# Performance work log

Hardware: AMD Instinct MI355X
Metric: run time of the kernel (lower is better)

Reference implementation:

```python
import jax, jax.numpy as jnp
import numpy as np
from jax import lax

CUTOFF = 0.25
SIGMA = 1.0
RADIUS = 4  # skimage/scipy default truncate=4.0 -> radius = round(4.0*sigma)


def _gauss_kernel(sigma=SIGMA, radius=RADIUS):
    x = np.arange(-radius, radius + 1, dtype=np.float32)
    k = np.exp(-0.5 * (x / sigma) ** 2)
    return jnp.asarray(k / k.sum())


def _blur_axis(x, axis, kernel):
    r = (kernel.shape[0] - 1) // 2
    pad = [(0, 0)] * x.ndim
    pad[axis] = (r, r)
    xp = jnp.pad(x, pad, mode='edge')  # scipy mode='nearest'
    out = jnp.zeros_like(x)
    for i in range(kernel.shape[0]):  # fixed small tap loop (9 taps)
        out = out + kernel[i] * lax.slice_in_dim(xp, i, i + x.shape[axis], axis=axis)
    return out


def gaussian_smoothing_4d(x):
    # skimage.filters.gaussian on a 4D array smooths over ALL axes (B, C, H, W)
    k = _gauss_kernel().astype(x.dtype)
    for ax in range(4):
        x = _blur_axis(x, ax, k)
    return x


def dht_2d(x):
    # real(FFT(x)) - imag(FFT(flip(x)))
    return (jnp.fft.fftn(x, axes=(2, 3)).real
            - jnp.fft.fftn(jnp.flip(x, axis=(2, 3)), axes=(2, 3)).imag).astype(x.dtype)


def _neg_k(a):
    # X_H(-k): flip both spatial mode axes, then roll by 1 (DC stays put)
    return jnp.roll(jnp.flip(a, axis=(-2, -1)), shift=(1, 1), axis=(-2, -1))


def compl_mul2d(x1, x2):
    x1n, x2n = _neg_k(x1), _neg_k(x2)
    e = lambda a, b: jnp.einsum('bixy,ioxy->boxy', a, b)
    return 0.5 * (e(x1, x2) - e(x1n, x2n) + e(x1, x2n) + e(x1n, x2))


def setup_inputs() -> dict:
    key = jax.random.key(0)
    k1, k2 = jax.random.split(key)
    B, Cin, Cout, H, W, M1, M2 = 16, 64, 64, 128, 128, 20, 20
    x = jax.random.normal(k1, (B, Cin, H, W), dtype=jnp.float32)
    scale = 1.0 / (Cin * Cout)
    w1 = scale * jax.random.uniform(k2, (Cin, Cout, M1, M2), dtype=jnp.float32)
    return {'x': x, 'w1': w1}


def reference(x, w1):
    B, _, H, W = x.shape
    Cout, M1, M2 = w1.shape[1], w1.shape[2], w1.shape[3]
    x_ht = dht_2d(x)
    out_ht = jnp.zeros((B, Cout, H, W), dtype=x.dtype)
    out_ht = out_ht.at[:, :, :M1, :M2].set(
        compl_mul2d(x_ht[:, :, :M1, :M2], w1))
    # inverse DHT = DHT / (H*W)
    y = dht_2d(out_ht) / (H * W)
    y = gaussian_smoothing_4d(y)
    # low-pass mask along last dim only (as in the original)
    freqs = jnp.fft.fftfreq(W)
    mask = (jnp.abs(freqs) <= CUTOFF).astype(y.dtype)
    return y * mask
```

## Files before the change

### kernel.cpp

```cpp
#include <hip/hip_runtime.h>


#define TWO_PI 6.283185307179586f
#define THETA (TWO_PI / 128.0f)

__device__ __forceinline__ void gauss9(float* g) {
  float s = 0.f;
#pragma unroll
  for (int t = 0; t < 9; ++t) { float d = (float)(t - 4); g[t] = expf(-0.5f * d * d); s += g[t]; }
  float inv = 1.f / s;
#pragma unroll
  for (int t = 0; t < 9; ++t) g[t] *= inv;
}

__global__ void __launch_bounds__(256, 4) kBig(
    const float* __restrict__ x, const float* __restrict__ w1,
    float* __restrict__ X1, float* __restrict__ wbT,
    float* __restrict__ L2g, float* __restrict__ RB2g) {
  __shared__ float lds[10240];
  int tid = threadIdx.x;
  int blk = blockIdx.x;

  if (blk < 448) {
    int c = blk / 7, chunk = blk % 7;
    int m0 = chunk * 64;
    int mw = 400 - m0; if (mw > 64) mw = 64;
    for (int t = tid; t < 4096; t += 256) {
      int o = t >> 6, mm = t & 63;
      lds[o * 69 + mm] = (mm < mw) ? w1[(c * 64 + o) * 400 + m0 + mm] : 0.f;
    }
    __syncthreads();
    float g[9]; gauss9(g);
    for (int t = tid; t < 4096; t += 256) {
      int mm = t >> 6, o = t & 63;
      if (mm >= mw) continue;
      float acc = 0.f;
#pragma unroll
      for (int tp = 0; tp < 9; ++tp) {
        int oc = o - 4 + tp; oc = oc < 0 ? 0 : (oc > 63 ? 63 : oc);
        acc += g[tp] * lds[oc * 69 + mm];
      }
      wbT[(c * 400 + m0 + mm) * 64 + o] = acc;
    }
    return;
  }
  if (blk == 448) {
    for (int i = tid; i < 5376; i += 256) {
      int u = i / 42, t = i - u * 42;
      int A = (t < 21) ? t : t - 21;
      float a = (float)((u * A) & 127) * THETA;
      lds[u * 44 + t] = (t < 21) ? cosf(a) : sinf(a);
    }
    __syncthreads();
    float g[9]; gauss9(g);
    for (int i = tid; i < 5376; i += 256) {
      int u = i / 42, t = i - u * 42;
      float acc = 0.f;
#pragma unroll
      for (int tp = 0; tp < 9; ++tp) {
        int uc = u - 4 + tp; uc = uc < 0 ? 0 : (uc > 127 ? 127 : uc);
        acc += g[tp] * lds[uc * 44 + t];
      }
      L2g[t * 128 + u] = acc;
      bool keep = (u <= 32) || (u >= 96);
      RB2g[t * 128 + u] = keep ? acc : 0.f;
    }
    return;
  }

  int bc0 = (blk - 449) * 2;
  const float* xb0 = x + (long)bc0 * 16384;
  const float* xb1 = xb0 + 16384;

  for (int i = tid; i < 2560; i += 256) {
    int n2 = i / 20, k2 = i - n2 * 20;
    float s, c;
    sincosf((float)((k2 * n2) & 127) * THETA, &s, &c);
    lds[n2 * 40 + k2] = c;
    lds[n2 * 40 + 20 + k2] = s;
  }

  int rg = tid & 31, cg = tid >> 5;
  int r0 = rg * 4, c0 = cg * 5;
  float acc0[4][5], acc1[4][5];
#pragma unroll
  for (int i = 0; i < 4; ++i)
#pragma unroll
    for (int j = 0; j < 5; ++j) { acc0[i][j] = 0.f; acc1[i][j] = 0.f; }

  float* xs0 = lds + 5120;
  float* xs1 = lds + 7232;
  for (int ch = 0; ch < 8; ++ch) {
    __syncthreads();
#pragma unroll 4
    for (int it = 0; it < 4; ++it) {
      int t = tid + it * 256;
      int n2l = t & 15, n1g = (t >> 4) & 31, im = t >> 9;
      const float* gp = (im ? xb1 : xb0) + n1g * 512 + ch * 16 + n2l;
      float4 v = make_float4(gp[0], gp[128], gp[256], gp[384]);
      float* dst = im ? xs1 : xs0;
      *(float4*)&dst[n2l * 132 + n1g * 4] = v;
    }
    __syncthreads();
#pragma unroll 4
    for (int k = 0; k < 16; ++k) {
      float4 a0 = *(const float4*)&xs0[k * 132 + r0];
      float4 a1 = *(const float4*)&xs1[k * 132 + r0];
      const float* tr = lds + (ch * 16 + k) * 40 + c0;
      float bv[5] = {tr[0], tr[1], tr[2], tr[3], tr[4]};
      float a0v[4] = {a0.x, a0.y, a0.z, a0.w};
      float a1v[4] = {a1.x, a1.y, a1.z, a1.w};
#pragma unroll
      for (int i = 0; i < 4; ++i)
#pragma unroll
        for (int j = 0; j < 5; ++j) {
          acc0[i][j] += a0v[i] * bv[j];
          acc1[i][j] += a1v[i] * bv[j];
        }
    }
  }
  __syncthreads();
  for (int i = tid; i < 2560; i += 256) {
    int k1 = i >> 7, t = i & 127;
    float s, c;
    sincosf((float)((k1 * t) & 127) * THETA, &s, &c);
    lds[k1 * 128 + (t ^ ((k1 & 7) << 2))] = c;
    lds[(20 + k1) * 128 + (t ^ (((20 + k1) & 7) << 2))] = s;
  }
#pragma unroll
  for (int j = 0; j < 5; ++j) {
    int col = c0 + j;
    int k2 = (col < 20) ? col : col - 20;
    int part = (col < 20) ? 0 : 128;
    int m = (k2 & 7) << 2;
    *(float4*)&lds[5120 + k2 * 256 + ((part + r0) ^ m)] =
        make_float4(acc0[0][j], acc0[1][j], acc0[2][j], acc0[3][j]);
  }
  __syncthreads();
  if (tid < 200) {
    int k1 = tid / 10, k2 = (tid % 10) * 2;
    int mc = (k1 & 7) << 2, ms = ((20 + k1) & 7) << 2;
    int m0 = (k2 & 7) << 2, m1 = ((k2 + 1) & 7) << 2;
    const float* tgc = lds + k1 * 128;
    const float* tgs = lds + (20 + k1) * 128;
    const float* p0 = lds + 5120 + k2 * 256;
    const float* p1 = lds + 5120 + (k2 + 1) * 256;
    float Ac0 = 0.f, As0 = 0.f, Bc0 = 0.f, Bs0 = 0.f;
    float Ac1 = 0.f, As1 = 0.f, Bc1 = 0.f, Bs1 = 0.f;
    for (int t = 0; t < 128; t += 4) {
      float4 tc = *(const float4*)(tgc + (t ^ mc));
      float4 ts = *(const float4*)(tgs + (t ^ ms));
      float4 pc0 = *(const float4*)(p0 + (t ^ m0));
      float4 ps0 = *(const float4*)(p0 + 128 + (t ^ m0));
      float4 pc1 = *(const float4*)(p1 + (t ^ m1));
      float4 ps1 = *(const float4*)(p1 + 128 + (t ^ m1));
      Ac0 += tc.x*pc0.x + tc.y*pc0.y + tc.z*pc0.z + tc.w*pc0.w;
      As0 += ts.x*pc0.x + ts.y*pc0.y + ts.z*pc0.z + ts.w*pc0.w;
      Bc0 += tc.x*ps0.x + tc.y*ps0.y + tc.z*ps0.z + tc.w*ps0.w;
      Bs0 += ts.x*ps0.x + ts.y*ps0.y + ts.z*ps0.z + ts.w*ps0.w;
      Ac1 += tc.x*pc1.x + tc.y*pc1.y + tc.z*pc1.z + tc.w*pc1.w;
      As1 += ts.x*pc1.x + ts.y*pc1.y + ts.z*pc1.z + ts.w*pc1.w;
      Bc1 += tc.x*ps1.x + tc.y*ps1.y + tc.z*ps1.z + tc.w*ps1.w;
      Bs1 += ts.x*ps1.x + ts.y*ps1.y + ts.z*ps1.z + ts.w*ps1.w;
    }
    float sa, ca, sb, cb;
    sincosf(THETA * (float)(k1 + k2), &sa, &ca);
    sincosf(THETA * (float)(k1 + k2 + 1), &sb, &cb);
    X1[(k1 * 20 + k2) * 1024 + bc0] = (Ac0 - Bs0) * (1.f - sa) - (As0 + Bc0) * ca;
    X1[(k1 * 20 + k2 + 1) * 1024 + bc0] = (Ac1 - Bs1) * (1.f - sb) - (As1 + Bc1) * cb;
  }
  __syncthreads();
#pragma unroll
  for (int j = 0; j < 5; ++j) {
    int col = c0 + j;
    int k2 = (col < 20) ? col : col - 20;
    int part = (col < 20) ? 0 : 128;
    int m = (k2 & 7) << 2;
    *(float4*)&lds[5120 + k2 * 256 + ((part + r0) ^ m)] =
        make_float4(acc1[0][j], acc1[1][j], acc1[2][j], acc1[3][j]);
  }
  __syncthreads();
  if (tid < 200) {
    int k1 = tid / 10, k2 = (tid % 10) * 2;
    int mc = (k1 & 7) << 2, ms = ((20 + k1) & 7) << 2;
    int m0 = (k2 & 7) << 2, m1 = ((k2 + 1) & 7) << 2;
    const float* tgc = lds + k1 * 128;
    const float* tgs = lds + (20 + k1) * 128;
    const float* p0 = lds + 5120 + k2 * 256;
    const float* p1 = lds + 5120 + (k2 + 1) * 256;
    float Ac0 = 0.f, As0 = 0.f, Bc0 = 0.f, Bs0 = 0.f;
    float Ac1 = 0.f, As1 = 0.f, Bc1 = 0.f, Bs1 = 0.f;
    for (int t = 0; t < 128; t += 4) {
      float4 tc = *(const float4*)(tgc + (t ^ mc));
      float4 ts = *(const float4*)(tgs + (t ^ ms));
      float4 pc0 = *(const float4*)(p0 + (t ^ m0));
      float4 ps0 = *(const float4*)(p0 + 128 + (t ^ m0));
      float4 pc1 = *(const float4*)(p1 + (t ^ m1));
      float4 ps1 = *(const float4*)(p1 + 128 + (t ^ m1));
      Ac0 += tc.x*pc0.x + tc.y*pc0.y + tc.z*pc0.z + tc.w*pc0.w;
      As0 += ts.x*pc0.x + ts.y*pc0.y + ts.z*pc0.z + ts.w*pc0.w;
      Bc0 += tc.x*ps0.x + tc.y*ps0.y + tc.z*ps0.z + tc.w*ps0.w;
      Bs0 += ts.x*ps0.x + ts.y*ps0.y + ts.z*ps0.z + ts.w*ps0.w;
      Ac1 += tc.x*pc1.x + tc.y*pc1.y + tc.z*pc1.z + tc.w*pc1.w;
      As1 += ts.x*pc1.x + ts.y*pc1.y + ts.z*pc1.z + ts.w*pc1.w;
      Bc1 += tc.x*ps1.x + tc.y*ps1.y + tc.z*ps1.z + tc.w*ps1.w;
      Bs1 += ts.x*ps1.x + ts.y*ps1.y + ts.z*ps1.z + ts.w*ps1.w;
    }
    float sa, ca, sb, cb;
    sincosf(THETA * (float)(k1 + k2), &sa, &ca);
    sincosf(THETA * (float)(k1 + k2 + 1), &sb, &cb);
    int bc1 = bc0 + 1;
    X1[(k1 * 20 + k2) * 1024 + bc1] = (Ac0 - Bs0) * (1.f - sa) - (As0 + Bc0) * ca;
    X1[(k1 * 20 + k2 + 1) * 1024 + bc1] = (Ac1 - Bs1) * (1.f - sb) - (As1 + Bc1) * cb;
  }
}

__global__ void k3_mix(const float* __restrict__ X1, const float* __restrict__ wbT,
                       float* __restrict__ O) {
  __shared__ float Xp[16][64], Xm[16][64];
  int m = blockIdx.x;
  int i = m / 20, j = m - i * 20;
  int nm = ((20 - i) % 20) * 20 + ((20 - j) % 20);
  int tid = threadIdx.x;
  const float sc = 0.5f / 16384.0f;
  float g[9]; gauss9(g);
  {
    int bl = tid >> 6, c = tid & 63;
#pragma unroll
    for (int it = 0; it < 4; ++it) {
      int b = bl * 4 + it;
      float sa = 0.f, sn = 0.f;
#pragma unroll
      for (int tp = 0; tp < 9; ++tp) {
        int bb = b - 4 + tp; bb = bb < 0 ? 0 : (bb > 15 ? 15 : bb);
        sa += g[tp] * X1[m * 1024 + bb * 64 + c];
        sn += g[tp] * X1[nm * 1024 + bb * 64 + c];
      }
      Xp[b][c] = (sa + sn) * sc; Xm[b][c] = (sa - sn) * sc;
    }
  }
  __syncthreads();
  int o = tid & 63, bq = tid >> 6;
  float acc[4] = {0.f, 0.f, 0.f, 0.f};
#pragma unroll 4
  for (int c = 0; c < 64; ++c) {
    float wp = wbT[(c * 400 + m) * 64 + o];
    float wm = wbT[(c * 400 + nm) * 64 + o];
#pragma unroll
    for (int k = 0; k < 4; ++k)
      acc[k] += Xp[bq * 4 + k][c] * wp + Xm[bq * 4 + k][c] * wm;
  }
#pragma unroll
  for (int k = 0; k < 4; ++k)
    O[((bq * 4 + k) * 64 + o) * 400 + m] = acc[k];
}

__global__ void __launch_bounds__(256) k5b_final(const float* __restrict__ O,
                                                 const float* __restrict__ L2g,
                                                 const float* __restrict__ RB2g,
                                                 float* __restrict__ out) {
  __shared__ float Os[400];
  __shared__ float Rs[42 * 128];
  int bo = blockIdx.x, tid = threadIdx.x;
  for (int t = tid; t < 400; t += 256) Os[t] = O[bo * 400 + t];
  __syncthreads();
  const float4* Bc4 = (const float4*)RB2g;
  const float4* Bs4 = (const float4*)(RB2g + 21 * 128);
  {
    int rg = tid & 7;
    int vqIdx = tid >> 3;
    int vq = (vqIdx < 9) ? vqIdx : vqIdx + 15;
    if (rg < 7 && vqIdx < 17) {
      int r0 = rg * 6;
      float4 a[6];
#pragma unroll
      for (int q = 0; q < 6; ++q) a[q] = make_float4(0.f, 0.f, 0.f, 0.f);
      for (int k2 = 0; k2 <= 20; ++k2) {
        float4 bc4 = Bc4[k2 * 32 + vq];
        float4 bs4 = Bs4[k2 * 32 + vq];
#pragma unroll
        for (int q = 0; q < 6; ++q) {
          int r = r0 + q;
          bool isS = (r >= 21);
          int A = isS ? (r - 21) : r;
          if (k2 < 20 && A < 20) {
            float ov = Os[A * 20 + k2];
            const float4 b = isS ? bs4 : bc4;
            float s = isS ? -ov : ov;
            a[q].x += s * b.x; a[q].y += s * b.y; a[q].z += s * b.z; a[q].w += s * b.w;
          }
          if (k2 >= 1 && A >= 1) {
            float ov = Os[(A - 1) * 20 + (k2 - 1)];
            const float4 b = isS ? bc4 : bs4;
            a[q].x -= ov * b.x; a[q].y -= ov * b.y; a[q].z -= ov * b.z; a[q].w -= ov * b.w;
          }
        }
      }
#pragma unroll
      for (int q = 0; q < 6; ++q)
        *(float4*)&Rs[(r0 + q) * 128 + vq * 4] = a[q];
    }
  }
  __syncthreads();
  long base = (long)bo * 16384;
  {
    int half = tid >> 7;
    int uu = (tid >> 3) & 15;  int u0 = uu * 8;
    int vv = tid & 7;          int v0 = half ? (96 + vv * 4) : vv * 4;
    float acc[8][4];
#pragma unroll
    for (int a = 0; a < 8; ++a)
#pragma unroll
      for (int b = 0; b < 4; ++b) acc[a][b] = 0.f;
    for (int r = 0; r < 42; ++r) {
      float4 a0 = *(const float4*)(L2g + r * 128 + u0);
      float4 a1 = *(const float4*)(L2g + r * 128 + u0 + 4);
      float4 b0 = *(const float4*)&Rs[r * 128 + v0];
      float av[8] = {a0.x, a0.y, a0.z, a0.w, a1.x, a1.y, a1.z, a1.w};
      float bv[4] = {b0.x, b0.y, b0.z, b0.w};
#pragma unroll
      for (int a = 0; a < 8; ++a)
#pragma unroll
        for (int b = 0; b < 4; ++b) acc[a][b] += av[a] * bv[b];
    }
#pragma unroll
    for (int a = 0; a < 8; ++a)
      *(float4*)&out[base + (u0 + a) * 128 + v0] =
          make_float4(acc[a][0], acc[a][1], acc[a][2], acc[a][3]);
  }
  if (tid < 128) {
    float d = 0.f;
    for (int r = 0; r < 42; ++r) d += L2g[r * 128 + tid] * Rs[r * 128 + 32];
    out[base + tid * 128 + 32] = d;
  }
  float4 z4 = make_float4(0.f, 0.f, 0.f, 0.f);
  for (int jj = tid; jj < 2048; jj += 256) {
    int u = jj >> 4, s = jj & 15;
    long p = base + (long)u * 128;
    if (s == 15) { out[p + 33] = 0.f; out[p + 34] = 0.f; out[p + 35] = 0.f; }
    else *(float4*)&out[p + 36 + 4 * s] = z4;
  }
}

extern "C" void kernel_launch(void* const* d_in, const int* in_sizes, int n_in,
                              void* d_out, int out_size, void* d_ws, size_t ws_size,
                              hipStream_t stream) {
  const float* x = (const float*)d_in[0];
  const float* w1 = (const float*)d_in[1];
  float* out = (float*)d_out;
  float* ws = (float*)d_ws;

  float* X1 = ws;
  float* O = X1 + 409600;
  float* wbT = O + 409600;
  float* L2g = wbT + 1638400;
  float* RB2g = L2g + 5376;

  hipLaunchKernelGGL(kBig, dim3(961), dim3(256), 0, stream,
                     x, w1, X1, wbT, L2g, RB2g);
  hipLaunchKernelGGL(k3_mix, dim3(400), dim3(256), 0, stream, X1, wbT, O);
  hipLaunchKernelGGL(k5b_final, dim3(1024), dim3(256), 0, stream, O, L2g, RB2g, out);
}
```

Before: 187.9 us.

## Prefetch next input chunk into registers and move setup blocks to grid end

Global loads of the next 16-column x chunk now go into registers while the current chunk is computed, a software pipeline that hides load latency behind the FMA loop. The weight-blur and trig-table setup blocks are moved from the start of the grid to block indices at 512 and above, so the main DFT blocks get scheduled first. This costs extra registers (four float4 values), which may reduce occupancy. The launch grid must match the new index mapping.

```diff
diff --git a/kernel.cpp b/kernel.cpp
--- a/kernel.cpp
+++ b/kernel.cpp
@@ -21,8 +21,32 @@
   int tid = threadIdx.x;
   int blk = blockIdx.x;
 
-  if (blk < 448) {
-    int c = blk / 7, chunk = blk % 7;
+  if (blk >= 512) {
+    if (blk == 960) {
+      for (int i = tid; i < 5376; i += 256) {
+        int u = i / 42, t = i - u * 42;
+        int A = (t < 21) ? t : t - 21;
+        float a = (float)((u * A) & 127) * THETA;
+        lds[u * 44 + t] = (t < 21) ? cosf(a) : sinf(a);
+      }
+      __syncthreads();
+      float g[9]; gauss9(g);
+      for (int i = tid; i < 5376; i += 256) {
+        int u = i / 42, t = i - u * 42;
+        float acc = 0.f;
+#pragma unroll
+        for (int tp = 0; tp < 9; ++tp) {
+          int uc = u - 4 + tp; uc = uc < 0 ? 0 : (uc > 127 ? 127 : uc);
+          acc += g[tp] * lds[uc * 44 + t];
+        }
+        L2g[t * 128 + u] = acc;
+        bool keep = (u <= 32) || (u >= 96);
+        RB2g[t * 128 + u] = keep ? acc : 0.f;
+      }
+      return;
+    }
+    int bb = blk - 512;
+    int c = bb / 7, chunk = bb % 7;
     int m0 = chunk * 64;
     int mw = 400 - m0; if (mw > 64) mw = 64;
     for (int t = tid; t < 4096; t += 256) {
@@ -44,33 +68,19 @@
     }
     return;
   }
-  if (blk == 448) {
-    for (int i = tid; i < 5376; i += 256) {
-      int u = i / 42, t = i - u * 42;
-      int A = (t < 21) ? t : t - 21;
-      float a = (float)((u * A) & 127) * THETA;
-      lds[u * 44 + t] = (t < 21) ? cosf(a) : sinf(a);
-    }
-    __syncthreads();
-    float g[9]; gauss9(g);
-    for (int i = tid; i < 5376; i += 256) {
-      int u = i / 42, t = i - u * 42;
-      float acc = 0.f;
-#pragma unroll
-      for (int tp = 0; tp < 9; ++tp) {
-        int uc = u - 4 + tp; uc = uc < 0 ? 0 : (uc > 127 ? 127 : uc);
-        acc += g[tp] * lds[uc * 44 + t];
-      }
-      L2g[t * 128 + u] = acc;
-      bool keep = (u <= 32) || (u >= 96);
-      RB2g[t * 128 + u] = keep ? acc : 0.f;
-    }
-    return;
-  }
-
-  int bc0 = (blk - 449) * 2;
+
+  int bc0 = blk * 2;
   const float* xb0 = x + (long)bc0 * 16384;
   const float* xb1 = xb0 + 16384;
+
+  float4 pv[4];
+#pragma unroll
+  for (int it = 0; it < 4; ++it) {
+    int t = tid + it * 256;
+    int n2l = t & 15, n1g = (t >> 4) & 31, im = t >> 9;
+    const float* gp = (im ? xb1 : xb0) + n1g * 512 + n2l;
+    pv[it] = make_float4(gp[0], gp[128], gp[256], gp[384]);
+  }
 
   for (int i = tid; i < 2560; i += 256) {
     int n2 = i / 20, k2 = i - n2 * 20;
@@ -92,14 +102,21 @@
   float* xs1 = lds + 7232;
   for (int ch = 0; ch < 8; ++ch) {
     __syncthreads();
-#pragma unroll 4
+#pragma unroll
     for (int it = 0; it < 4; ++it) {
       int t = tid + it * 256;
       int n2l = t & 15, n1g = (t >> 4) & 31, im = t >> 9;
-      const float* gp = (im ? xb1 : xb0) + n1g * 512 + ch * 16 + n2l;
-      float4 v = make_float4(gp[0], gp[128], gp[256], gp[384]);
       float* dst = im ? xs1 : xs0;
-      *(float4*)&dst[n2l * 132 + n1g * 4] = v;
+      *(float4*)&dst[n2l * 132 + n1g * 4] = pv[it];
+    }
+    if (ch < 7) {
+#pragma unroll
+      for (int it = 0; it < 4; ++it) {
+        int t = tid + it * 256;
+        int n2l = t & 15, n1g = (t >> 4) & 31, im = t >> 9;
+        const float* gp = (im ? xb1 : xb0) + n1g * 512 + (ch + 1) * 16 + n2l;
+        pv[it] = make_float4(gp[0], gp[128], gp[256], gp[384]);
+      }
     }
     __syncthreads();
 #pragma unroll 4
```

Result: faster. 181.5 us (-3.4%).
